# Kernel tuning notes

Measured on AMD Instinct MI355X. Metric: run time of the kernel, lower is better.

The kernel has to match this reference:

```python
import jax, jax.numpy as jnp
import numpy as np

N_NODES = 50000
N_EDGES = 800000
IN_CH = 128
MEAN_SIZE = 128
VAR_SIZE = 128


def setup_inputs() -> dict:
    key = jax.random.key(0)
    k_x, k_e, k_wm, k_wv = jax.random.split(key, 4)
    x = jax.random.normal(k_x, (N_NODES, IN_CH), dtype=jnp.float32)
    edge_index = jax.random.randint(k_e, (2, N_EDGES), 0, N_NODES, dtype=jnp.int32)
    # torch Linear(2*C, M, bias=False) weight has shape [M, 2*C]
    s = 1.0 / np.sqrt(2 * IN_CH)
    w_mean = jax.random.uniform(k_wm, (MEAN_SIZE, 2 * IN_CH), jnp.float32, -s, s)
    w_var = jax.random.uniform(k_wv, (VAR_SIZE, 2 * IN_CH), jnp.float32, -s, s)
    return {"x": x, "edge_index": edge_index, "w_mean": w_mean, "w_var": w_var}


def reference(x, edge_index, w_mean, w_var):
    row, col = edge_index[0], edge_index[1]
    x_row = x[row]  # [E, C]
    x_col = x[col]  # [E, C]
    # cat([x_row, x_col], 1) @ W.T  ==  x_row @ W[:, :C].T + x_col @ W[:, C:].T
    C = x.shape[1]
    maps_mean = jnp.einsum('ec,mc->em', x_row, w_mean[:, :C]) + \
                jnp.einsum('ec,mc->em', x_col, w_mean[:, C:])
    maps_var = jnp.einsum('ec,vc->ev', x_row, w_var[:, :C]) + \
               jnp.einsum('ec,vc->ev', x_col, w_var[:, C:])
    return (maps_mean, maps_var)
```

## Files before the change

kernel.cpp:

```cpp
#include <hip/hip_runtime.h>
#include <hip/hip_bf16.h>

#define NODES 50000
#define EDGES 800000
#define CH 128
#define NCOL 512
#define MPAD 50048
#define EPW 8
#define NB 196
#define BINBLK 256
#define CHUNK 3125

typedef __attribute__((ext_vector_type(8))) __bf16 bf16x8;
typedef __attribute__((ext_vector_type(4))) float f32x4;
typedef unsigned long long u64;

static __device__ __forceinline__ unsigned short f2bf(float f) {
    union { float f; unsigned u; } v; v.f = f;
    unsigned r = v.u + 0x7FFFu + ((v.u >> 16) & 1u);
    return (unsigned short)(r >> 16);
}
static __device__ __forceinline__ float bf2f(unsigned short h) {
    union { unsigned u; float f; } v; v.u = ((unsigned)h) << 16;
    return v.f;
}

__global__ void k_cvt_x(const float* __restrict__ x, unsigned short* __restrict__ xb) {
    int i = blockIdx.x * blockDim.x + threadIdx.x;
    if (i >= MPAD * CH / 4) return;
    int base = i << 2;
    unsigned short s0 = 0, s1 = 0, s2 = 0, s3 = 0;
    if (base < NODES * CH) {
        const f32x4 v = *reinterpret_cast<const f32x4*>(x + base);
        s0 = f2bf(v[0]); s1 = f2bf(v[1]); s2 = f2bf(v[2]); s3 = f2bf(v[3]);
    }
    u64 p = (u64)s0 | ((u64)s1 << 16) | ((u64)s2 << 32) | ((u64)s3 << 48);
    *reinterpret_cast<u64*>(xb + base) = p;
}

__global__ void k_pack_w(const float* __restrict__ wm, const float* __restrict__ wv,
                         unsigned short* __restrict__ wb) {
    int i = blockIdx.x * blockDim.x + threadIdx.x;
    if (i >= NCOL * CH) return;
    int n = i >> 7, k = i & 127;
    float v;
    if (n < 128)      v = wm[n * 256 + k];
    else if (n < 256) v = wv[(n - 128) * 256 + k];
    else if (n < 384) v = wm[(n - 256) * 256 + 128 + k];
    else              v = wv[(n - 384) * 256 + 128 + k];
    wb[i] = f2bf(v);
}

__global__ __launch_bounds__(256) void k_gemm(const unsigned short* __restrict__ xb,
                                              const unsigned short* __restrict__ wb,
                                              unsigned short* __restrict__ th) {
    const int lane = threadIdx.x & 63;
    const int wave = threadIdx.x >> 6;
    const int rowbase = blockIdx.x * 128 + (wave >> 1) * 64;
    const int colbase = blockIdx.y * 128 + (wave & 1) * 64;
    const int lr = lane & 15;
    const int kg = lane >> 4;
    f32x4 acc[4][4] = {};
#pragma unroll
    for (int ks = 0; ks < 4; ++ks) {
        const int k = ks * 32 + kg * 8;
        bf16x8 af[4], bfr[4];
#pragma unroll
        for (int a = 0; a < 4; ++a)
            af[a] = *reinterpret_cast<const bf16x8*>(xb + (size_t)(rowbase + a * 16 + lr) * CH + k);
#pragma unroll
        for (int b = 0; b < 4; ++b)
            bfr[b] = *reinterpret_cast<const bf16x8*>(wb + (size_t)(colbase + b * 16 + lr) * CH + k);
#pragma unroll
        for (int a = 0; a < 4; ++a)
#pragma unroll
            for (int b = 0; b < 4; ++b)
                acc[a][b] = __builtin_amdgcn_mfma_f32_16x16x32_bf16(af[a], bfr[b], acc[a][b], 0, 0, 0);
    }
    const int crow = (lane >> 4) * 4;
    const int ccol = lane & 15;
#pragma unroll
    for (int a = 0; a < 4; ++a)
#pragma unroll
        for (int b = 0; b < 4; ++b)
#pragma unroll
            for (int j = 0; j < 4; ++j) {
                int row = rowbase + a * 16 + crow + j;
                int col = colbase + b * 16 + ccol;
                th[(size_t)row * NCOL + col] = f2bf(acc[a][b][j]);
            }
}

__global__ void k_zero(unsigned* __restrict__ hist) {
    if (threadIdx.x < 256) hist[threadIdx.x] = 0;
}

__global__ __launch_bounds__(256) void k_binA(const int* __restrict__ ei,
                                              unsigned* __restrict__ hist,
                                              unsigned* __restrict__ blockOff) {
    __shared__ unsigned h[NB];
    for (int t = threadIdx.x; t < NB; t += 256) h[t] = 0;
    __syncthreads();
    const int base = blockIdx.x * CHUNK;
    for (int i = threadIdx.x; i < CHUNK; i += 256)
        atomicAdd(&h[((unsigned)ei[base + i]) >> 8], 1u);
    __syncthreads();
    for (int t = threadIdx.x; t < NB; t += 256)
        blockOff[blockIdx.x * NB + t] = atomicAdd(&hist[t], h[t]);
}

__global__ void k_scan(const unsigned* __restrict__ hist, unsigned* __restrict__ basearr) {
    __shared__ unsigned v[256];
    int t = threadIdx.x;
    unsigned mine = (t < NB) ? hist[t] : 0;
    v[t] = mine;
    __syncthreads();
    for (int off = 1; off < 256; off <<= 1) {
        unsigned x = (t >= off) ? v[t - off] : 0;
        __syncthreads();
        v[t] += x;
        __syncthreads();
    }
    if (t < NB) basearr[t] = v[t] - mine;
}

__global__ __launch_bounds__(256) void k_binB(const int* __restrict__ ei,
                                              const unsigned* __restrict__ basearr,
                                              const unsigned* __restrict__ blockOff,
                                              u64* __restrict__ binned) {
    __shared__ unsigned cur[NB];
    for (int t = threadIdx.x; t < NB; t += 256) cur[t] = 0;
    __syncthreads();
    const int base = blockIdx.x * CHUNK;
    for (int i = threadIdx.x; i < CHUNK; i += 256) {
        int e = base + i;
        unsigned r = (unsigned)ei[e];
        unsigned c = (unsigned)ei[EDGES + e];
        unsigned b = r >> 8;
        unsigned rank = atomicAdd(&cur[b], 1u);
        unsigned pos = basearr[b] + blockOff[blockIdx.x * NB + b] + rank;
        binned[pos] = (u64)r | ((u64)c << 17) | ((u64)e << 34);
    }
}

__global__ __launch_bounds__(256) void k_edges_b(const u64* __restrict__ binned,
                                                 const unsigned short* __restrict__ th,
                                                 float* __restrict__ out) {
    const int wave = threadIdx.x >> 6;
    const int lane = threadIdx.x & 63;
    const int half = lane >> 5;
    const int l = lane & 31;
    const int ebase = (blockIdx.x * 4 + wave) * EPW;

    u64 rec[EPW];
#pragma unroll
    for (int i = 0; i < EPW; ++i) rec[i] = binned[ebase + i];
    u64 pa[EPW], pb[EPW];
#pragma unroll
    for (int i = 0; i < EPW; ++i) {
        const unsigned r = (unsigned)(rec[i] & 0x1FFFF);
        const unsigned c = (unsigned)((rec[i] >> 17) & 0x1FFFF);
        pa[i] = *reinterpret_cast<const u64*>(th + (size_t)r * NCOL + half * 128 + l * 4);
        pb[i] = *reinterpret_cast<const u64*>(th + (size_t)c * NCOL + 256 + half * 128 + l * 4);
    }
    const size_t obase = (size_t)half * ((size_t)EDGES * 128) + (size_t)l * 4;
#pragma unroll
    for (int i = 0; i < EPW; ++i) {
        const unsigned e = (unsigned)(rec[i] >> 34);
        f32x4 s;
        s[0] = bf2f((unsigned short)pa[i])         + bf2f((unsigned short)pb[i]);
        s[1] = bf2f((unsigned short)(pa[i] >> 16)) + bf2f((unsigned short)(pb[i] >> 16));
        s[2] = bf2f((unsigned short)(pa[i] >> 32)) + bf2f((unsigned short)(pb[i] >> 32));
        s[3] = bf2f((unsigned short)(pa[i] >> 48)) + bf2f((unsigned short)(pb[i] >> 48));
        __builtin_nontemporal_store(
            s, reinterpret_cast<f32x4*>(out + obase + (size_t)e * 128));
    }
}

__global__ __launch_bounds__(256) void k_edges(const int* __restrict__ ei,
                                               const unsigned short* __restrict__ th,
                                               float* __restrict__ out) {
    const int wave = threadIdx.x >> 6;
    const int lane = threadIdx.x & 63;
    const int half = lane >> 5;
    const int l = lane & 31;
    const int ebase = (blockIdx.x * 4 + wave) * EPW;
    int rr[EPW], cc[EPW];
#pragma unroll
    for (int i = 0; i < EPW; ++i) { rr[i] = ei[ebase + i]; cc[i] = ei[EDGES + ebase + i]; }
    u64 pa[EPW], pb[EPW];
#pragma unroll
    for (int i = 0; i < EPW; ++i) {
        pa[i] = *reinterpret_cast<const u64*>(th + (size_t)rr[i] * NCOL + half * 128 + l * 4);
        pb[i] = *reinterpret_cast<const u64*>(th + (size_t)cc[i] * NCOL + 256 + half * 128 + l * 4);
    }
    const size_t obase = (size_t)half * ((size_t)EDGES * 128) + (size_t)l * 4;
#pragma unroll
    for (int i = 0; i < EPW; ++i) {
        f32x4 s;
        s[0] = bf2f((unsigned short)pa[i])         + bf2f((unsigned short)pb[i]);
        s[1] = bf2f((unsigned short)(pa[i] >> 16)) + bf2f((unsigned short)(pb[i] >> 16));
        s[2] = bf2f((unsigned short)(pa[i] >> 32)) + bf2f((unsigned short)(pb[i] >> 32));
        s[3] = bf2f((unsigned short)(pa[i] >> 48)) + bf2f((unsigned short)(pb[i] >> 48));
        __builtin_nontemporal_store(
            s, reinterpret_cast<f32x4*>(out + obase + (size_t)(ebase + i) * 128));
    }
}

__global__ void k_naive(const float* __restrict__ x, const int* __restrict__ ei,
                        const float* __restrict__ wm, const float* __restrict__ wv,
                        float* __restrict__ out) {
    __shared__ float xs[256];
    int e = blockIdx.x;
    int t = threadIdx.x;
    int r = ei[e], c = ei[EDGES + e];
    xs[t] = (t < 128) ? x[(size_t)r * 128 + t] : x[(size_t)c * 128 + (t - 128)];
    __syncthreads();
    const float* w = (t < 128) ? (wm + (size_t)t * 256) : (wv + (size_t)(t - 128) * 256);
    float acc = 0.f;
#pragma unroll 8
    for (int k = 0; k < 256; ++k) acc = fmaf(xs[k], w[k], acc);
    size_t ooff = (t < 128) ? ((size_t)e * 128 + t)
                            : ((size_t)EDGES * 128 + (size_t)e * 128 + (t - 128));
    out[ooff] = acc;
}

extern "C" void kernel_launch(void* const* d_in, const int* in_sizes, int n_in,
                              void* d_out, int out_size, void* d_ws, size_t ws_size,
                              hipStream_t stream) {
    const float* x  = (const float*)d_in[0];
    const int*   ei = (const int*)d_in[1];
    const float* wm = (const float*)d_in[2];
    const float* wv = (const float*)d_in[3];
    float* out = (float*)d_out;

    const size_t xb_b   = (size_t)MPAD * CH * 2;
    const size_t wb_b   = (size_t)NCOL * CH * 2;
    const size_t th_b   = (size_t)MPAD * NCOL * 2;
    const size_t hist_b = 1024;
    const size_t base_b = 1024;
    const size_t boff_b = (size_t)BINBLK * NB * 4;
    const size_t bin_b  = (size_t)EDGES * 8;

    const size_t need_tab = xb_b + wb_b + th_b;
    const size_t need_bin = need_tab + hist_b + base_b + boff_b + bin_b;

    if (ws_size < need_tab) {
        k_naive<<<EDGES, 256, 0, stream>>>(x, ei, wm, wv, out);
        return;
    }

    char* w0 = (char*)d_ws;
    unsigned short* xb  = (unsigned short*)w0;
    unsigned short* wb  = (unsigned short*)(w0 + xb_b);
    unsigned short* tab = (unsigned short*)(w0 + xb_b + wb_b);

    k_cvt_x<<<(MPAD * CH / 4 + 255) / 256, 256, 0, stream>>>(x, xb);
    k_pack_w<<<(NCOL * CH + 255) / 256, 256, 0, stream>>>(wm, wv, wb);
    dim3 g(MPAD / 128, NCOL / 128);
    k_gemm<<<g, 256, 0, stream>>>(xb, wb, tab);

    if (ws_size >= need_bin) {
        unsigned* hist    = (unsigned*)(w0 + need_tab);
        unsigned* basearr = (unsigned*)(w0 + need_tab + hist_b);
        unsigned* boff    = (unsigned*)(w0 + need_tab + hist_b + base_b);
        u64*      binned  = (u64*)    (w0 + need_tab + hist_b + base_b + boff_b);
        k_zero<<<1, 256, 0, stream>>>(hist);
        k_binA<<<BINBLK, 256, 0, stream>>>(ei, hist, boff);
        k_scan<<<1, 256, 0, stream>>>(hist, basearr);
        k_binB<<<BINBLK, 256, 0, stream>>>(ei, basearr, boff, binned);
        k_edges_b<<<EDGES / (4 * EPW), 256, 0, stream>>>(binned, tab, out);
    } else {
        k_edges<<<EDGES / (4 * EPW), 256, 0, stream>>>(ei, tab, out);
    }
}
```

Before: 267.3 us.

## Bin edges by 2D (row, col) node blocks to improve gather locality

```diff
diff --git a/kernel.cpp b/kernel.cpp
--- a/kernel.cpp
+++ b/kernel.cpp
@@ -7,7 +7,8 @@
 #define NCOL 512
 #define MPAD 50048
 #define EPW 8
-#define NB 196
+#define NRB 98
+#define NBK (NRB * NRB)
 #define BINBLK 256
 #define CHUNK 3125
 
@@ -92,53 +93,55 @@
 }
 
 __global__ void k_zero(unsigned* __restrict__ hist) {
-    if (threadIdx.x < 256) hist[threadIdx.x] = 0;
+    int i = blockIdx.x * blockDim.x + threadIdx.x;
+    if (i < NBK) hist[i] = 0;
 }
 
 __global__ __launch_bounds__(256) void k_binA(const int* __restrict__ ei,
-                                              unsigned* __restrict__ hist,
-                                              unsigned* __restrict__ blockOff) {
-    __shared__ unsigned h[NB];
-    for (int t = threadIdx.x; t < NB; t += 256) h[t] = 0;
+                                              unsigned* __restrict__ hist) {
+    __shared__ unsigned h[NBK];
+    for (int t = threadIdx.x; t < NBK; t += 256) h[t] = 0;
     __syncthreads();
     const int base = blockIdx.x * CHUNK;
-    for (int i = threadIdx.x; i < CHUNK; i += 256)
-        atomicAdd(&h[((unsigned)ei[base + i]) >> 8], 1u);
-    __syncthreads();
-    for (int t = threadIdx.x; t < NB; t += 256)
-        blockOff[blockIdx.x * NB + t] = atomicAdd(&hist[t], h[t]);
-}
-
-__global__ void k_scan(const unsigned* __restrict__ hist, unsigned* __restrict__ basearr) {
-    __shared__ unsigned v[256];
-    int t = threadIdx.x;
-    unsigned mine = (t < NB) ? hist[t] : 0;
-    v[t] = mine;
+    for (int i = threadIdx.x; i < CHUNK; i += 256) {
+        unsigned r = (unsigned)ei[base + i];
+        unsigned c = (unsigned)ei[EDGES + base + i];
+        atomicAdd(&h[(r >> 9) * NRB + (c >> 9)], 1u);
+    }
+    __syncthreads();
+    for (int t = threadIdx.x; t < NBK; t += 256)
+        if (h[t]) atomicAdd(&hist[t], h[t]);
+}
+
+__global__ __launch_bounds__(256) void k_scan(const unsigned* __restrict__ hist,
+                                              unsigned* __restrict__ cursor) {
+    __shared__ unsigned part[256];
+    const int t = threadIdx.x;
+    const int per = (NBK + 255) / 256;
+    const int lo = t * per, hi = min(NBK, lo + per);
+    unsigned s = 0;
+    for (int i = lo; i < hi; ++i) s += hist[i];
+    part[t] = s;
     __syncthreads();
     for (int off = 1; off < 256; off <<= 1) {
-        unsigned x = (t >= off) ? v[t - off] : 0;
+        unsigned x = (t >= off) ? part[t - off] : 0;
         __syncthreads();
-        v[t] += x;
+        part[t] += x;
         __syncthreads();
     }
-    if (t < NB) basearr[t] = v[t] - mine;
+    unsigned run = part[t] - s;
+    for (int i = lo; i < hi; ++i) { cursor[i] = run; run += hist[i]; }
 }
 
 __global__ __launch_bounds__(256) void k_binB(const int* __restrict__ ei,
-                                              const unsigned* __restrict__ basearr,
-                                              const unsigned* __restrict__ blockOff,
+                                              unsigned* __restrict__ cursor,
                                               u64* __restrict__ binned) {
-    __shared__ unsigned cur[NB];
-    for (int t = threadIdx.x; t < NB; t += 256) cur[t] = 0;
-    __syncthreads();
     const int base = blockIdx.x * CHUNK;
     for (int i = threadIdx.x; i < CHUNK; i += 256) {
         int e = base + i;
         unsigned r = (unsigned)ei[e];
         unsigned c = (unsigned)ei[EDGES + e];
-        unsigned b = r >> 8;
-        unsigned rank = atomicAdd(&cur[b], 1u);
-        unsigned pos = basearr[b] + blockOff[blockIdx.x * NB + b] + rank;
+        unsigned pos = atomicAdd(&cursor[(r >> 9) * NRB + (c >> 9)], 1u);
         binned[pos] = (u64)r | ((u64)c << 17) | ((u64)e << 34);
     }
 }
@@ -237,13 +240,12 @@
     const size_t xb_b   = (size_t)MPAD * CH * 2;
     const size_t wb_b   = (size_t)NCOL * CH * 2;
     const size_t th_b   = (size_t)MPAD * NCOL * 2;
-    const size_t hist_b = 1024;
-    const size_t base_b = 1024;
-    const size_t boff_b = (size_t)BINBLK * NB * 4;
+    const size_t hist_b = (size_t)NBK * 4;
+    const size_t cur_b  = (size_t)NBK * 4;
     const size_t bin_b  = (size_t)EDGES * 8;
 
     const size_t need_tab = xb_b + wb_b + th_b;
-    const size_t need_bin = need_tab + hist_b + base_b + boff_b + bin_b;
+    const size_t need_bin = need_tab + hist_b + cur_b + bin_b;
 
     if (ws_size < need_tab) {
         k_naive<<<EDGES, 256, 0, stream>>>(x, ei, wm, wv, out);
@@ -261,14 +263,13 @@
     k_gemm<<<g, 256, 0, stream>>>(xb, wb, tab);
 
     if (ws_size >= need_bin) {
-        unsigned* hist    = (unsigned*)(w0 + need_tab);
-        unsigned* basearr = (unsigned*)(w0 + need_tab + hist_b);
-        unsigned* boff    = (unsigned*)(w0 + need_tab + hist_b + base_b);
-        u64*      binned  = (u64*)    (w0 + need_tab + hist_b + base_b + boff_b);
-        k_zero<<<1, 256, 0, stream>>>(hist);
-        k_binA<<<BINBLK, 256, 0, stream>>>(ei, hist, boff);
-        k_scan<<<1, 256, 0, stream>>>(hist, basearr);
-        k_binB<<<BINBLK, 256, 0, stream>>>(ei, basearr, boff, binned);
+        unsigned* hist   = (unsigned*)(w0 + need_tab);
+        unsigned* cursor = (unsigned*)(w0 + need_tab + hist_b);
+        u64*      binned = (u64*)    (w0 + need_tab + hist_b + cur_b);
+        k_zero<<<(NBK + 255) / 256, 256, 0, stream>>>(hist);
+        k_binA<<<BINBLK, 256, 0, stream>>>(ei, hist);
+        k_scan<<<1, 256, 0, stream>>>(hist, cursor);
+        k_binB<<<BINBLK, 256, 0, stream>>>(ei, cursor, binned);
         k_edges_b<<<EDGES / (4 * EPW), 256, 0, stream>>>(binned, tab, out);
     } else {
         k_edges<<<EDGES / (4 * EPW), 256, 0, stream>>>(ei, tab, out);
```

New measurement: 330.9 us. +23.8%, slower.
